# Performance work log

Hardware: AMD Instinct MI355X
Metric: run time of the kernel (lower is better)

The kernel has to match this reference:

```python
import jax, jax.numpy as jnp
import numpy as np

B, T, H, L = 8, 256, 64, 3
NB, NF, HP = 17, 68, 6
K = 9  # temporal kernel
PAD = (K - 1) // 2
EPS = 1e-5


def _normalize(adj):
    adj = adj + np.eye(adj.shape[0], dtype=np.float32)
    d = adj.sum(1)
    dinv = np.power(d, -0.5)
    dinv[np.isinf(dinv)] = 0.0
    return (dinv[:, None] * adj * dinv[None, :]).astype(np.float32)


def _body_adj():
    a = np.zeros((NB, NB), np.float32)
    conns = [(0, 1), (0, 2), (1, 3), (2, 4), (0, 5), (0, 6), (5, 6), (5, 7), (7, 9), (6, 8), (8, 10), (5, 11), (6, 12), (11, 12), (11, 13), (13, 15), (12, 14), (14, 16)]
    for i, j in conns:
        a[i, j] = 1.0
        a[j, i] = 1.0
    return _normalize(a)


def _face_adj():
    a = np.zeros((NF, NF), np.float32)
    for i in range(16): a[i, i + 1] = 1.0
    for i in range(17, 21): a[i, i + 1] = 1.0
    for i in range(22, 26): a[i, i + 1] = 1.0
    for i in range(27, 30): a[i, i + 1] = 1.0
    for i in range(31, 35): a[i, i + 1] = 1.0
    for i in range(36, 41): a[i, i + 1] = 1.0
    a[41, 36] = 1.0
    for i in range(42, 47): a[i, i + 1] = 1.0
    a[47, 42] = 1.0
    for i in range(48, 59): a[i, i + 1] = 1.0
    a[59, 48] = 1.0
    for i in range(60, 67): a[i, i + 1] = 1.0
    a[67, 60] = 1.0
    a = a + a.T
    return _normalize(a)


def setup_inputs() -> dict:
    keys = iter(jax.random.split(jax.random.key(0), 80))

    def rn(shape, s):
        return jax.random.normal(next(keys), shape, jnp.float32) * s

    inp = {}
    inp['body_kps'] = jax.random.normal(next(keys), (B, T, NB * 2), jnp.float32)
    inp['face_kps_2d'] = jax.random.normal(next(keys), (B, T, NF * 2), jnp.float32)
    inp['head_pose'] = jax.random.normal(next(keys), (B, T, HP), jnp.float32)
    inp['body_adj'] = jnp.asarray(_body_adj())
    inp['face_adj'] = jnp.asarray(_face_adj())
    inp['body_proj_w'] = rn((2, H), 0.5)
    inp['body_proj_b'] = jnp.zeros((H,), jnp.float32)
    inp['face_proj_w'] = rn((2, H), 0.5)
    inp['face_proj_b'] = jnp.zeros((H,), jnp.float32)
    inp['head_w'] = rn((HP, H), 0.3)
    inp['head_b'] = jnp.zeros((H,), jnp.float32)
    for p in ('b', 'f'):
        inp[p + '_t1w'] = rn((L, H, H, K), 0.04)
        inp[p + '_t1b'] = jnp.zeros((L, H), jnp.float32)
        inp[p + '_bn1g'] = jnp.ones((L, H), jnp.float32)
        inp[p + '_bn1b'] = jnp.zeros((L, H), jnp.float32)
        inp[p + '_bn1m'] = rn((L, H), 0.1)
        inp[p + '_bn1v'] = jax.random.uniform(next(keys), (L, H), jnp.float32, 0.5, 1.5)
        inp[p + '_gcw'] = rn((L, H, H), 0.1)
        inp[p + '_gcb'] = jnp.zeros((L, H), jnp.float32)
        inp[p + '_t2w'] = rn((L, H, H, K), 0.04)
        inp[p + '_t2b'] = jnp.zeros((L, H), jnp.float32)
        inp[p + '_bn2g'] = jnp.ones((L, H), jnp.float32)
        inp[p + '_bn2b'] = jnp.zeros((L, H), jnp.float32)
        inp[p + '_bn2m'] = rn((L, H), 0.1)
        inp[p + '_bn2v'] = jax.random.uniform(next(keys), (L, H), jnp.float32, 0.5, 1.5)
    total = NB * H + NF * H + H  # 5504
    inp['fus1_w'] = rn((total, 4 * H), 0.02)
    inp['fus1_b'] = jnp.zeros((4 * H,), jnp.float32)
    inp['fus2_w'] = rn((4 * H, 2 * H), 0.06)
    inp['fus2_b'] = jnp.zeros((2 * H,), jnp.float32)
    inp['fus3_w'] = rn((2 * H, H), 0.09)
    inp['fus3_b'] = jnp.zeros((H,), jnp.float32)
    inp['fus4_w'] = rn((H, 5), 0.12)
    inp['fus4_b'] = jnp.zeros((5,), jnp.float32)
    return inp


def _conv_bn(x, w, b, g, be, m, v):
    # x: (BN, C, T); w: (O, I, K). Conv1d (pad=4) + eval-mode BatchNorm1d.
    y = jax.lax.conv_general_dilated(x, w, (1,), [(PAD, PAD)], dimension_numbers=('NCH', 'OIH', 'NCH'))
    y = y + b[None, :, None]
    inv = g * jax.lax.rsqrt(v + EPS)
    return y * inv[None, :, None] + (be - m * inv)[None, :, None]


def _block(x, adj, t1w, t1b, g1, b1, m1, v1, gw, gb, t2w, t2b, g2, b2, m2, v2):
    # x: (B, N, C, T); residual is identity (in_channels == out_channels)
    Bn, N, C, Tn = x.shape
    res = x
    h = jax.nn.relu(_conv_bn(x.reshape(Bn * N, C, Tn), t1w, t1b, g1, b1, m1, v1)).reshape(Bn, N, C, Tn)
    # spatial graph conv, batched over all timesteps at once (adj @ (x W) + b)
    support = jnp.einsum('bnct,co->bnot', h, gw)
    h = jax.nn.relu(jnp.einsum('mn,bnot->bmot', adj, support) + gb[None, None, :, None])
    h = _conv_bn(h.reshape(Bn * N, C, Tn), t2w, t2b, g2, b2, m2, v2).reshape(Bn, N, C, Tn)
    return h + res  # dropout = identity in eval


def _stream(x, n_nodes, pw, pb, adj, ps):
    Bn, Tn, _ = x.shape
    h = x.reshape(Bn, Tn, n_nodes, 2) @ pw + pb          # (B, T, N, H)
    h = jnp.transpose(h, (0, 2, 3, 1))                   # (B, N, H, T)
    for l in range(ps[0].shape[0]):
        h = _block(h, adj, *(p[l] for p in ps))
    return h.mean(axis=3).reshape(Bn, -1)                # temporal mean-pool, flatten nodes


def reference(body_kps, face_kps_2d, head_pose, body_adj, face_adj, body_proj_w, body_proj_b, face_proj_w, face_proj_b, head_w, head_b, b_t1w, b_t1b, b_bn1g, b_bn1b, b_bn1m, b_bn1v, b_gcw, b_gcb, b_t2w, b_t2b, b_bn2g, b_bn2b, b_bn2m, b_bn2v, f_t1w, f_t1b, f_bn1g, f_bn1b, f_bn1m, f_bn1v, f_gcw, f_gcb, f_t2w, f_t2b, f_bn2g, f_bn2b, f_bn2m, f_bn2v, fus1_w, fus1_b, fus2_w, fus2_b, fus3_w, fus3_b, fus4_w, fus4_b):
    bps = (b_t1w, b_t1b, b_bn1g, b_bn1b, b_bn1m, b_bn1v, b_gcw, b_gcb, b_t2w, b_t2b, b_bn2g, b_bn2b, b_bn2m, b_bn2v)
    fps = (f_t1w, f_t1b, f_bn1g, f_bn1b, f_bn1m, f_bn1v, f_gcw, f_gcb, f_t2w, f_t2b, f_bn2g, f_bn2b, f_bn2m, f_bn2v)
    bf = _stream(body_kps, NB, body_proj_w, body_proj_b, body_adj, bps)
    ff = _stream(face_kps_2d, NF, face_proj_w, face_proj_b, face_adj, fps)
    hp = jax.nn.relu(head_pose @ head_w + head_b).mean(axis=1)
    feat = jnp.concatenate([bf, ff, hp], axis=-1)
    h = jax.nn.relu(feat @ fus1_w + fus1_b)
    h = jax.nn.relu(h @ fus2_w + fus2_b)
    h = jax.nn.relu(h @ fus3_w + fus3_b)
    return h @ fus4_w + fus4_b
```

## Files before the change

kernel.cpp:

```cpp
#include <hip/hip_runtime.h>

constexpr int B_ = 8, T_ = 256, H_ = 64, L_ = 3, NB_ = 17, NF_ = 68, HP_ = 6, K_ = 9;
constexpr int FEAT_DIM = NB_ * H_ + NF_ * H_ + H_;
constexpr int HT = H_ * T_;

typedef _Float16 half4_t __attribute__((ext_vector_type(4)));
typedef _Float16 half8_t __attribute__((ext_vector_type(8)));
typedef float f32x16 __attribute__((ext_vector_type(16)));
typedef float f32x4 __attribute__((ext_vector_type(4)));

constexpr size_t SZ_AB = (size_t)B_ * NB_ * HT;
constexpr size_t SZ_AF = (size_t)B_ * NF_ * HT;
constexpr size_t OFF_TB   = 0;
constexpr size_t OFF_TF   = OFF_TB + SZ_AB / 2;
constexpr size_t OFF_SUPB = OFF_TF + SZ_AF / 2;
constexpr size_t OFF_SUPF = OFF_SUPB + SZ_AB / 2;
constexpr size_t OFF_GB   = OFF_SUPF + SZ_AF / 2;
constexpr size_t OFF_GF   = OFF_GB + SZ_AB / 2;
constexpr size_t OFF_W3   = OFF_GF + SZ_AF / 2;
constexpr size_t OFF_GW3  = OFF_W3 + 4 * 55296;
constexpr size_t OFF_B2   = OFF_GW3 + 2 * 6144;
constexpr size_t OFF_ADJPB= OFF_B2 + 768;
constexpr size_t OFF_ADJPF= OFF_ADJPB + 512;
constexpr size_t OFF_FEAT = OFF_ADJPF + 3840;
constexpr size_t OFF_P1   = OFF_FEAT + (size_t)B_ * FEAT_DIM;

struct ConvPrepSet { const float *w, *tb, *g, *bb, *m, *v; };

struct Args {
    const float *body_kps, *face_kps, *head_pose, *body_adj, *face_adj;
    const float *body_pw, *body_pb, *face_pw, *face_pb, *head_w, *head_b;
    ConvPrepSet sb1, sb2, sf1, sf2;
    const float *b_gcw, *f_gcw, *b_gcb, *f_gcb;
    const float *fus1_w, *fus1_b, *fus2_w, *fus2_b, *fus3_w, *fus3_b, *fus4_w, *fus4_b;
    _Float16 *TrB, *TrF, *SupB, *SupF, *Gb, *Gf;
    _Float16 *W3, *GW3, *adjPB, *adjPF;
    float *B2, *p1, *feat;
    float *out;
};

__device__ __forceinline__ half8_t ld_b8(const _Float16* p) {
    half4_t lo = *(const half4_t*)p;
    half4_t hi = *(const half4_t*)(p + 4);
    return __builtin_shufflevector(lo, hi, 0, 1, 2, 3, 4, 5, 6, 7);
}

__device__ __forceinline__ void st_b8(_Float16* p, half8_t v) {
    half4_t lo, hi;
#pragma unroll
    for (int j = 0; j < 4; ++j) { lo[j] = v[j]; hi[j] = v[4 + j]; }
    *(half4_t*)p = lo;
    *(half4_t*)(p + 4) = hi;
}

__device__ __forceinline__ void stage_chunk64(const _Float16* __restrict__ xb,
                                              _Float16* __restrict__ Xs, int tc, int tid) {
    for (int u = tid; u < 72 * 8; u += 256) {
        int row = u >> 3, c = u & 7;
        int t = tc * 64 + row - 4;
        half8_t v;
        if (t >= 0 && t < T_) {
            v = *(const half8_t*)(xb + (size_t)t * H_ + c * 8);
        } else {
#pragma unroll
            for (int j = 0; j < 8; ++j) v[j] = (_Float16)0.f;
        }
        st_b8(&Xs[row * 68 + c * 8], v);
    }
}

__device__ __forceinline__ void stage_res64(const _Float16* __restrict__ xb,
                                            _Float16* __restrict__ Rs, int tc, int tid) {
    for (int u = tid; u < 64 * 8; u += 256) {
        int row = u >> 3, c = u & 7;
        half8_t v = *(const half8_t*)(xb + (size_t)(tc * 64 + row) * H_ + c * 8);
        st_b8(&Rs[row * 68 + c * 8], v);
    }
}

__device__ __forceinline__ void conv_kloop(const half8_t* __restrict__ wl,
                                           const _Float16* __restrict__ Xs,
                                           int trow, int ln31, int kg, int ot,
                                           f32x16& acc) {
    const _Float16* xr0 = Xs + (size_t)(trow + ln31) * 68;
#pragma unroll
    for (int tap = 0; tap < K_; ++tap) {
#pragma unroll
        for (int ks = 0; ks < 4; ++ks) {
            int i8 = ks * 2 + kg;
            half8_t a = wl[(tap * 8 + i8) * H_ + ot * 32 + ln31];
            half8_t bf = ld_b8(xr0 + tap * 68 + i8 * 8);
            acc = __builtin_amdgcn_mfma_f32_32x32x16_f16(a, bf, acc, 0, 0, 0);
        }
    }
}

__device__ void convmix_core(const half8_t* __restrict__ wl,
                             const float* __restrict__ b1l,
                             const half8_t* __restrict__ gl,
                             _Float16* __restrict__ supb,
                             int tc, _Float16* __restrict__ Xs, int tid) {
    int ln = tid & 63;
    int w = __builtin_amdgcn_readfirstlane(tid >> 6);
    int ln31 = ln & 31, kg = ln >> 5;
    int ts = w & 1, ot = w >> 1;
    int trow = ts * 32;

    f32x16 acc;
#pragma unroll
    for (int r = 0; r < 16; ++r) acc[r] = 0.f;

    conv_kloop(wl, Xs, trow, ln31, kg, ot, acc);
    __syncthreads();

    _Float16* mrow = Xs + (size_t)(4 + trow + ln31) * 68;
#pragma unroll
    for (int rg = 0; rg < 4; ++rg) {
        int o0 = ot * 32 + rg * 8 + kg * 4;
        f32x4 bv = *(const f32x4*)(b1l + o0);
        half4_t hv;
#pragma unroll
        for (int j = 0; j < 4; ++j)
            hv[j] = (_Float16)fmaxf(acc[rg * 4 + j] + bv[j], 0.f);
        *(half4_t*)(mrow + o0) = hv;
    }
    __syncthreads();

    f32x16 acc2;
#pragma unroll
    for (int r = 0; r < 16; ++r) acc2[r] = 0.f;
#pragma unroll
    for (int ks = 0; ks < 4; ++ks) {
        int i8 = ks * 2 + kg;
        half8_t a = gl[i8 * H_ + ot * 32 + ln31];
        half8_t bf = ld_b8(mrow + i8 * 8);
        acc2 = __builtin_amdgcn_mfma_f32_32x32x16_f16(a, bf, acc2, 0, 0, 0);
    }
    __syncthreads();

#pragma unroll
    for (int rg = 0; rg < 4; ++rg) {
        int o0 = ot * 32 + rg * 8 + kg * 4;
        half4_t hv;
#pragma unroll
        for (int j = 0; j < 4; ++j)
            hv[j] = (_Float16)acc2[rg * 4 + j];
        *(half4_t*)(mrow + o0) = hv;
    }
    __syncthreads();
    _Float16* gout = supb + (size_t)(tc * 64) * H_;
    const _Float16* srow = Xs + 4 * 68;
#pragma unroll
    for (int k2 = 0; k2 < 2; ++k2) {
        int u = k2 * 256 + tid;
        int r = u >> 3, c = u & 7;
        half8_t v = ld_b8(srow + r * 68 + c * 8);
        *(half8_t*)(gout + (size_t)r * H_ + c * 8) = v;
    }
}

__global__ __launch_bounds__(256) void prep_k(Args A) {
    int blk = blockIdx.x;
    int tid = threadIdx.x;
    if (blk < 1728) {
        int set = blk / 432;
        int bx = blk % 432;
        ConvPrepSet s = (set == 0) ? A.sb1 : (set == 1) ? A.sb2 : (set == 2) ? A.sf1 : A.sf2;
        int idx = bx * 256 + tid;
        int k = idx % K_; int r = idx / K_;
        int i = r % H_; r /= H_;
        int o = r % H_; int l = r / H_;
        float sc = s.g[l * H_ + o] * rsqrtf(s.v[l * H_ + o] + 1e-5f);
        A.W3[(size_t)set * 110592 + ((((l * K_ + k) * 8 + (i >> 3)) * H_ + o) * 8) + (i & 7)]
            = (_Float16)(s.w[idx] * sc);
        if (i == 0 && k == 0)
            A.B2[set * 192 + l * H_ + o] =
                s.tb[l * H_ + o] * sc + s.bb[l * H_ + o] - s.m[l * H_ + o] * sc;
    } else if (blk < 1824) {
        int set = (blk - 1728) / 48;
        int bx = (blk - 1728) % 48;
        const float* gw = set ? A.f_gcw : A.b_gcw;
        int idx = bx * 256 + tid;
        int o = idx % H_; int r = idx / H_;
        int c = r % H_; int l = r / H_;
        A.GW3[(size_t)set * 12288 + (((l * 8 + (c >> 3)) * H_ + o) * 8) + (c & 7)]
            = (_Float16)gw[idx];
    } else {
        int idx = (blk - 1824) * 256 + tid;
        if (idx < 1024) {
            int m = idx >> 5, k = idx & 31;
            A.adjPB[idx] = (m < NB_ && k < NB_) ? (_Float16)A.body_adj[m * NB_ + k] : (_Float16)0.f;
        } else if (idx < 8704) {
            int j = idx - 1024;
            int m = j / 80, k = j % 80;
            A.adjPF[j] = (m < NF_ && k < NF_) ? (_Float16)A.face_adj[m * NF_ + k] : (_Float16)0.f;
        } else if (idx < 10752) {
            A.p1[idx - 8704] = 0.f;
        } else if (idx < 10752 + B_ * FEAT_DIM) {
            A.feat[idx - 10752] = 0.f;
        }
    }
}

__global__ __launch_bounds__(256, 8) void projcm_k(Args A) {
    __shared__ __align__(16) _Float16 Xs[72 * 68];
    int blk = blockIdx.x, tid = threadIdx.x;
    bool isB = blk < 4 * B_ * NB_;
    int j = isB ? blk : blk - 4 * B_ * NB_;
    int bn = j >> 2, tc = j & 3;
    const float* kps = isB ? A.body_kps : A.face_kps;
    const float* pw  = isB ? A.body_pw  : A.face_pw;
    const float* pb  = isB ? A.body_pb  : A.face_pb;
    _Float16* trunk  = isB ? A.TrB : A.TrF;
    int N = isB ? NB_ : NF_;
    int b = bn / N, n = bn % N;

    if (tid < 144) {
        int row = tid >> 1, hf = tid & 1;
        int t = tc * 64 + row - 4;
        _Float16* xr = Xs + row * 68 + hf * 32;
        if (t >= 0 && t < T_) {
            float x0 = kps[((size_t)b * T_ + t) * (N * 2) + n * 2 + 0];
            float x1 = kps[((size_t)b * T_ + t) * (N * 2) + n * 2 + 1];
            bool own = (row >= 4 && row < 68);
            _Float16* ob = trunk + (size_t)bn * HT + (size_t)t * H_ + hf * 32;
#pragma unroll
            for (int cg2 = 0; cg2 < 4; ++cg2) {
                half8_t v;
#pragma unroll
                for (int jj = 0; jj < 8; ++jj) {
                    int c = hf * 32 + cg2 * 8 + jj;
                    v[jj] = (_Float16)fmaf(x0, pw[c], fmaf(x1, pw[H_ + c], pb[c]));
                }
                st_b8(xr + cg2 * 8, v);
                if (own) *(half8_t*)(ob + cg2 * 8) = v;
            }
        } else {
            half8_t z;
#pragma unroll
            for (int jj = 0; jj < 8; ++jj) z[jj] = (_Float16)0.f;
            st_b8(xr, z);
            st_b8(xr + 8, z);
            st_b8(xr + 16, z);
            st_b8(xr + 24, z);
        }
    }
    __syncthreads();

    const half8_t* w1 = (const half8_t*)(A.W3 + (isB ? 0 : 221184));
    const float* b1l  = isB ? A.B2 : A.B2 + 384;
    const half8_t* gl = (const half8_t*)(A.GW3 + (isB ? 0 : 12288));
    _Float16* supb = (isB ? A.SupB : A.SupF) + (size_t)bn * HT;
    convmix_core(w1, b1l, gl, supb, tc, Xs, tid);
}

__global__ __launch_bounds__(256, 8) void cm_k(Args A, int l) {
    __shared__ __align__(16) _Float16 Xs[72 * 68];
    int blk = blockIdx.x, tid = threadIdx.x;
    bool isB = blk < 4 * B_ * NB_;
    int j = isB ? blk : blk - 4 * B_ * NB_;
    int bn = j >> 2, tc = j & 3;
    const _Float16* trunk = isB ? A.TrB : A.TrF;

    stage_chunk64(trunk + (size_t)bn * HT, Xs, tc, tid);
    __syncthreads();

    const half8_t* w1 = (const half8_t*)(A.W3 + (isB ? 0 : 221184)) + (size_t)l * (K_ * 8 * H_);
    const float* b1l  = (isB ? A.B2 : A.B2 + 384) + l * H_;
    const half8_t* gl = (const half8_t*)(A.GW3 + (isB ? 0 : 12288)) + (size_t)l * (8 * H_);
    _Float16* supb = (isB ? A.SupB : A.SupF) + (size_t)bn * HT;
    convmix_core(w1, b1l, gl, supb, tc, Xs, tid);
}

template <int N, int MT, int KS>
__device__ void adjmix_impl(const _Float16* __restrict__ sup,
                            const half8_t* __restrict__ adjP,
                            const float* __restrict__ gb,
                            _Float16* __restrict__ out,
                            int blk, int l, _Float16* Ls, int tid) {
    constexpr int KP = KS * 16;
    constexpr int PITCH = KP + 4;
    int b = blk >> 7, cb = blk & 127;
    int colbase = cb * 128;

    for (int u = tid; u < KP * 16; u += 256) {
        int n = u >> 4, cs = u & 15;
        half8_t v;
        if (n < N) v = *(const half8_t*)(sup + (size_t)(b * N + n) * HT + colbase + cs * 8);
        else {
#pragma unroll
            for (int j = 0; j < 8; ++j) v[j] = (_Float16)0.f;
        }
#pragma unroll
        for (int j = 0; j < 8; ++j) Ls[(cs * 8 + j) * PITCH + n] = v[j];
    }
    __syncthreads();

    int ln = tid & 63;
    int w = __builtin_amdgcn_readfirstlane(tid >> 6);
    int ln31 = ln & 31, kg = ln >> 5;
    int colL = w * 32 + ln31;

    f32x16 acc[MT];
#pragma unroll
    for (int mt = 0; mt < MT; ++mt)
#pragma unroll
        for (int r = 0; r < 16; ++r) acc[mt][r] = 0.f;

#pragma unroll
    for (int ks = 0; ks < KS; ++ks) {
        half8_t bf = ld_b8(&Ls[colL * PITCH + ks * 16 + kg * 8]);
#pragma unroll
        for (int mt = 0; mt < MT; ++mt) {
            half8_t af = adjP[(size_t)(mt * 32 + ln31) * (KP / 8) + ks * 2 + kg];
            acc[mt] = __builtin_amdgcn_mfma_f32_32x32x16_f16(af, bf, acc[mt], 0, 0, 0);
        }
    }
    __syncthreads();

    float gbv = gb[l * H_ + (colL & 63)];
#pragma unroll
    for (int mt = 0; mt < MT; ++mt) {
#pragma unroll
        for (int r = 0; r < 16; ++r) {
            int m = mt * 32 + (r & 3) + 8 * (r >> 2) + 4 * kg;
            Ls[m * 132 + colL] = (_Float16)fmaxf(acc[mt][r] + gbv, 0.f);
        }
    }
    __syncthreads();

    for (int u = tid; u < N * 16; u += 256) {
        int m = u >> 4, c = u & 15;
        half8_t v = ld_b8(&Ls[m * 132 + c * 8]);
        *(half8_t*)(out + (size_t)(b * N + m) * HT + colbase + c * 8) = v;
    }
}

__global__ __launch_bounds__(256) void adjmix_k(Args A, int l) {
    __shared__ __align__(16) _Float16 Ls[12800];
    int blk = blockIdx.x, tid = threadIdx.x;
    if (blk < 1024)
        adjmix_impl<NB_, 1, 2>(A.SupB, (const half8_t*)A.adjPB, A.b_gcb, A.Gb, blk, l, Ls, tid);
    else
        adjmix_impl<NF_, 3, 5>(A.SupF, (const half8_t*)A.adjPF, A.f_gcb, A.Gf, blk - 1024, l, Ls, tid);
}

__global__ __launch_bounds__(256, 8) void c2_k(Args A, int l) {
    __shared__ __align__(16) _Float16 Xs[72 * 68];
    __shared__ __align__(16) _Float16 Rs[64 * 68];
    int blk = blockIdx.x, tid = threadIdx.x;
    bool isB = blk < 4 * B_ * NB_;
    int j = isB ? blk : blk - 4 * B_ * NB_;
    int bn = j >> 2, tc = j & 3;
    const _Float16* G = isB ? A.Gb : A.Gf;
    _Float16* trunk   = isB ? A.TrB : A.TrF;
    const half8_t* w2 = (const half8_t*)(A.W3 + (isB ? 110592 : 331776)) + (size_t)l * (K_ * 8 * H_);
    const float* b2l  = (isB ? A.B2 + 192 : A.B2 + 576) + l * H_;

    stage_chunk64(G + (size_t)bn * HT, Xs, tc, tid);
    stage_res64(trunk + (size_t)bn * HT, Rs, tc, tid);
    __syncthreads();

    int ln = tid & 63;
    int w = __builtin_amdgcn_readfirstlane(tid >> 6);
    int ln31 = ln & 31, kg = ln >> 5;
    int ts = w & 1, ot = w >> 1;
    int trow = ts * 32;

    f32x16 acc;
#pragma unroll
    for (int r = 0; r < 16; ++r) acc[r] = 0.f;

    conv_kloop(w2, Xs, trow, ln31, kg, ot, acc);
    __syncthreads();

    {
        _Float16* orow = Xs + (size_t)(4 + trow + ln31) * 68;
        const _Float16* rrow = Rs + (size_t)(trow + ln31) * 68;
#pragma unroll
        for (int rg = 0; rg < 4; ++rg) {
            int o0 = ot * 32 + rg * 8 + kg * 4;
            f32x4 bv = *(const f32x4*)(b2l + o0);
            half4_t rv = *(const half4_t*)(rrow + o0);
            half4_t hv;
#pragma unroll
            for (int jj = 0; jj < 4; ++jj)
                hv[jj] = (_Float16)(acc[rg * 4 + jj] + bv[jj] + (float)rv[jj]);
            *(half4_t*)(orow + o0) = hv;
        }
    }
    __syncthreads();

    _Float16* gout = trunk + (size_t)bn * HT + (size_t)(tc * 64) * H_;
    const _Float16* srow = Xs + 4 * 68;
#pragma unroll
    for (int k2 = 0; k2 < 2; ++k2) {
        int u = k2 * 256 + tid;
        int r = u >> 3, c = u & 7;
        half8_t v = ld_b8(srow + r * 68 + c * 8);
        *(half8_t*)(gout + (size_t)r * H_ + c * 8) = v;
    }
}

__global__ __launch_bounds__(256, 8) void c2last_k(Args A) {
    __shared__ __align__(16) _Float16 Xs[72 * 68];
    __shared__ __align__(16) _Float16 Rs[64 * 68];
    int blk = blockIdx.x, tid = threadIdx.x;
    if (blk >= 2720) {
        int b = blk - 2720;
        if (tid < 64) {
            int c = tid;
            float w0 = A.head_w[c], w1 = A.head_w[64 + c], w2 = A.head_w[128 + c],
                  w3 = A.head_w[192 + c], w4 = A.head_w[256 + c], w5 = A.head_w[320 + c];
            float bias = A.head_b[c];
            float acc = 0.f;
            for (int t = 0; t < T_; ++t) {
                const float* xr = A.head_pose + ((size_t)b * T_ + t) * HP_;
                float s = fmaf(xr[0], w0, fmaf(xr[1], w1, fmaf(xr[2], w2,
                          fmaf(xr[3], w3, fmaf(xr[4], w4, fmaf(xr[5], w5, bias))))));
                acc += fmaxf(s, 0.f);
            }
            A.feat[(size_t)b * FEAT_DIM + NB_ * H_ + NF_ * H_ + c] = acc * (1.f / 256.f);
        }
        return;
    }
    constexpr int l = L_ - 1;
    bool isB = blk < 4 * B_ * NB_;
    int j = isB ? blk : blk - 4 * B_ * NB_;
    int bn = j >> 2, tc = j & 3;
    const _Float16* G = isB ? A.Gb : A.Gf;
    _Float16* trunk   = isB ? A.TrB : A.TrF;
    const half8_t* w2 = (const half8_t*)(A.W3 + (isB ? 110592 : 331776)) + (size_t)l * (K_ * 8 * H_);
    const float* b2l  = (isB ? A.B2 + 192 : A.B2 + 576) + l * H_;
    int N = isB ? NB_ : NF_;
    int fbase = isB ? 0 : NB_ * H_;

    stage_chunk64(G + (size_t)bn * HT, Xs, tc, tid);
    stage_res64(trunk + (size_t)bn * HT, Rs, tc, tid);
    __syncthreads();

    int ln = tid & 63;
    int w = __builtin_amdgcn_readfirstlane(tid >> 6);
    int ln31 = ln & 31, kg = ln >> 5;
    int ts = w & 1, ot = w >> 1;
    int trow = ts * 32;

    f32x16 acc;
#pragma unroll
    for (int r = 0; r < 16; ++r) acc[r] = 0.f;

    conv_kloop(w2, Xs, trow, ln31, kg, ot, acc);

    float sv[16];
    const _Float16* rrow = Rs + (size_t)(trow + ln31) * 68;
#pragma unroll
    for (int rg = 0; rg < 4; ++rg) {
        int o0 = ot * 32 + rg * 8 + kg * 4;
        f32x4 bv = *(const f32x4*)(b2l + o0);
        half4_t rv = *(const half4_t*)(rrow + o0);
#pragma unroll
        for (int jj = 0; jj < 4; ++jj) {
            int r = rg * 4 + jj;
            float s = acc[r] + bv[jj] + (float)rv[jj];
#pragma unroll
            for (int off = 1; off < 32; off <<= 1) s += __shfl_xor(s, off);
            sv[r] = s;
        }
    }
    __syncthreads();
    float* red = (float*)Xs;
    if (ln31 == 0) {
#pragma unroll
        for (int r = 0; r < 16; ++r) {
            int olocal = (r & 3) + 8 * (r >> 2) + 4 * kg;
            red[w * 32 + olocal] = sv[r];
        }
    }
    __syncthreads();
    if (tid < 64) {
        int o = tid, ot2 = o >> 5, ol = o & 31;
        float s = red[(ot2 * 2) * 32 + ol] + red[(ot2 * 2 + 1) * 32 + ol];
        int b = bn / N, n = bn % N;
        atomicAdd(&A.feat[(size_t)b * FEAT_DIM + fbase + n * H_ + o], s * (1.f / 256.f));
    }
}

__global__ __launch_bounds__(256) void fus1_k(Args A) {
    __shared__ float fv[8][64];
    int blk = blockIdx.x;
    int ic = blk >> 1, kh = blk & 1;
    int base = ic * 128 + kh * 64;
    int tid = threadIdx.x;
    for (int u = tid; u < 8 * 64; u += 256) {
        int b = u >> 6, j = u & 63;
        fv[b][j] = A.feat[(size_t)b * FEAT_DIM + base + j];
    }
    __syncthreads();
    float acc[8];
#pragma unroll
    for (int b = 0; b < 8; ++b) acc[b] = 0.f;
    const float* wb = A.fus1_w + (size_t)base * 256 + tid;
    for (int i = 0; i < 64; ++i) {
        float wv = wb[(size_t)i * 256];
#pragma unroll
        for (int b = 0; b < 8; ++b) acc[b] = fmaf(fv[b][i], wv, acc[b]);
    }
#pragma unroll
    for (int b = 0; b < 8; ++b) atomicAdd(&A.p1[b * 256 + tid], acc[b]);
}

__global__ __launch_bounds__(256) void fus_tail_k(Args A) {
    __shared__ float s1[256], s2[128], s3[64];
    int b = blockIdx.x, tid = threadIdx.x;
    s1[tid] = fmaxf(A.p1[b * 256 + tid] + A.fus1_b[tid], 0.f);
    __syncthreads();
    if (tid < 128) {
        float acc = A.fus2_b[tid];
        for (int i = 0; i < 256; ++i) acc = fmaf(s1[i], A.fus2_w[i * 128 + tid], acc);
        s2[tid] = fmaxf(acc, 0.f);
    }
    __syncthreads();
    if (tid < 64) {
        float acc = A.fus3_b[tid];
        for (int i = 0; i < 128; ++i) acc = fmaf(s2[i], A.fus3_w[i * 64 + tid], acc);
        s3[tid] = fmaxf(acc, 0.f);
    }
    __syncthreads();
    if (tid < 5) {
        float acc = A.fus4_b[tid];
        for (int i = 0; i < 64; ++i) acc = fmaf(s3[i], A.fus4_w[i * 5 + tid], acc);
        A.out[b * 5 + tid] = acc;
    }
}

extern "C" void kernel_launch(void* const* d_in, const int* in_sizes, int n_in,
                              void* d_out, int out_size, void* d_ws, size_t ws_size,
                              hipStream_t stream) {
    float* ws = (float*)d_ws;

    Args A;
    A.body_kps = (const float*)d_in[0];
    A.face_kps = (const float*)d_in[1];
    A.head_pose = (const float*)d_in[2];
    A.body_adj = (const float*)d_in[3];
    A.face_adj = (const float*)d_in[4];
    A.body_pw = (const float*)d_in[5];
    A.body_pb = (const float*)d_in[6];
    A.face_pw = (const float*)d_in[7];
    A.face_pb = (const float*)d_in[8];
    A.head_w = (const float*)d_in[9];
    A.head_b = (const float*)d_in[10];
    A.sb1 = ConvPrepSet{(const float*)d_in[11], (const float*)d_in[12], (const float*)d_in[13],
                        (const float*)d_in[14], (const float*)d_in[15], (const float*)d_in[16]};
    A.b_gcw = (const float*)d_in[17];
    A.b_gcb = (const float*)d_in[18];
    A.sb2 = ConvPrepSet{(const float*)d_in[19], (const float*)d_in[20], (const float*)d_in[21],
                        (const float*)d_in[22], (const float*)d_in[23], (const float*)d_in[24]};
    A.sf1 = ConvPrepSet{(const float*)d_in[25], (const float*)d_in[26], (const float*)d_in[27],
                        (const float*)d_in[28], (const float*)d_in[29], (const float*)d_in[30]};
    A.f_gcw = (const float*)d_in[31];
    A.f_gcb = (const float*)d_in[32];
    A.sf2 = ConvPrepSet{(const float*)d_in[33], (const float*)d_in[34], (const float*)d_in[35],
                        (const float*)d_in[36], (const float*)d_in[37], (const float*)d_in[38]};
    A.fus1_w = (const float*)d_in[39]; A.fus1_b = (const float*)d_in[40];
    A.fus2_w = (const float*)d_in[41]; A.fus2_b = (const float*)d_in[42];
    A.fus3_w = (const float*)d_in[43]; A.fus3_b = (const float*)d_in[44];
    A.fus4_w = (const float*)d_in[45]; A.fus4_b = (const float*)d_in[46];

    A.TrB  = (_Float16*)(ws + OFF_TB);
    A.TrF  = (_Float16*)(ws + OFF_TF);
    A.SupB = (_Float16*)(ws + OFF_SUPB);
    A.SupF = (_Float16*)(ws + OFF_SUPF);
    A.Gb   = (_Float16*)(ws + OFF_GB);
    A.Gf   = (_Float16*)(ws + OFF_GF);
    A.W3   = (_Float16*)(ws + OFF_W3);
    A.GW3  = (_Float16*)(ws + OFF_GW3);
    A.adjPB= (_Float16*)(ws + OFF_ADJPB);
    A.adjPF= (_Float16*)(ws + OFF_ADJPF);
    A.B2   = ws + OFF_B2;
    A.feat = ws + OFF_FEAT;
    A.p1   = ws + OFF_P1;
    A.out  = (float*)d_out;

    const int gconv = 4 * (B_ * NB_ + B_ * NF_);

    prep_k<<<2038, 256, 0, stream>>>(A);
    projcm_k<<<gconv, 256, 0, stream>>>(A);
    for (int l = 0; l < L_; ++l) {
        adjmix_k<<<2048, 256, 0, stream>>>(A, l);
        if (l < L_ - 1) {
            c2_k<<<gconv, 256, 0, stream>>>(A, l);
            cm_k<<<gconv, 256, 0, stream>>>(A, l + 1);
        } else {
            c2last_k<<<gconv + 8, 256, 0, stream>>>(A);
        }
    }
    fus1_k<<<86, 256, 0, stream>>>(A);
    fus_tail_k<<<8, 256, 0, stream>>>(A);
}
```

Baseline: 372.8 us.

## Fuse each GCN layer into one kernel using connected-component node groups

Replaces the separate conv+mix, dense adjacency-mix, and second-conv kernels with a single per-layer kernel. Each block owns a connected component of the skeleton or face graph (body, jaw, brows, nose, eyes, lips) for one batch and a 16-step time chunk, with halo rows for both temporal convs. The adjacency mix becomes a sparse neighbour sum in LDS instead of a padded dense MFMA. This removes global round trips for the support and graph-conv intermediates and several launches per layer. In exchange it adds redundant halo computation, uses a very large LDS allocation at one block per CU, and relies on the adjacency being block-diagonal across those fixed node groups.

```diff
diff --git a/kernel.cpp b/kernel.cpp
--- a/kernel.cpp
+++ b/kernel.cpp
@@ -13,16 +13,10 @@
 constexpr size_t SZ_AF = (size_t)B_ * NF_ * HT;
 constexpr size_t OFF_TB   = 0;
 constexpr size_t OFF_TF   = OFF_TB + SZ_AB / 2;
-constexpr size_t OFF_SUPB = OFF_TF + SZ_AF / 2;
-constexpr size_t OFF_SUPF = OFF_SUPB + SZ_AB / 2;
-constexpr size_t OFF_GB   = OFF_SUPF + SZ_AF / 2;
-constexpr size_t OFF_GF   = OFF_GB + SZ_AB / 2;
-constexpr size_t OFF_W3   = OFF_GF + SZ_AF / 2;
+constexpr size_t OFF_W3   = OFF_TF + SZ_AF / 2;
 constexpr size_t OFF_GW3  = OFF_W3 + 4 * 55296;
 constexpr size_t OFF_B2   = OFF_GW3 + 2 * 6144;
-constexpr size_t OFF_ADJPB= OFF_B2 + 768;
-constexpr size_t OFF_ADJPF= OFF_ADJPB + 512;
-constexpr size_t OFF_FEAT = OFF_ADJPF + 3840;
+constexpr size_t OFF_FEAT = OFF_B2 + 768;
 constexpr size_t OFF_P1   = OFF_FEAT + (size_t)B_ * FEAT_DIM;
 
 struct ConvPrepSet { const float *w, *tb, *g, *bb, *m, *v; };
@@ -33,8 +27,8 @@
     ConvPrepSet sb1, sb2, sf1, sf2;
     const float *b_gcw, *f_gcw, *b_gcb, *f_gcb;
     const float *fus1_w, *fus1_b, *fus2_w, *fus2_b, *fus3_w, *fus3_b, *fus4_w, *fus4_b;
-    _Float16 *TrB, *TrF, *SupB, *SupF, *Gb, *Gf;
-    _Float16 *W3, *GW3, *adjPB, *adjPF;
+    _Float16 *TrB, *TrF;
+    _Float16 *W3, *GW3;
     float *B2, *p1, *feat;
     float *out;
 };
@@ -51,112 +45,6 @@
     for (int j = 0; j < 4; ++j) { lo[j] = v[j]; hi[j] = v[4 + j]; }
     *(half4_t*)p = lo;
     *(half4_t*)(p + 4) = hi;
-}
-
-__device__ __forceinline__ void stage_chunk64(const _Float16* __restrict__ xb,
-                                              _Float16* __restrict__ Xs, int tc, int tid) {
-    for (int u = tid; u < 72 * 8; u += 256) {
-        int row = u >> 3, c = u & 7;
-        int t = tc * 64 + row - 4;
-        half8_t v;
-        if (t >= 0 && t < T_) {
-            v = *(const half8_t*)(xb + (size_t)t * H_ + c * 8);
-        } else {
-#pragma unroll
-            for (int j = 0; j < 8; ++j) v[j] = (_Float16)0.f;
-        }
-        st_b8(&Xs[row * 68 + c * 8], v);
-    }
-}
-
-__device__ __forceinline__ void stage_res64(const _Float16* __restrict__ xb,
-                                            _Float16* __restrict__ Rs, int tc, int tid) {
-    for (int u = tid; u < 64 * 8; u += 256) {
-        int row = u >> 3, c = u & 7;
-        half8_t v = *(const half8_t*)(xb + (size_t)(tc * 64 + row) * H_ + c * 8);
-        st_b8(&Rs[row * 68 + c * 8], v);
-    }
-}
-
-__device__ __forceinline__ void conv_kloop(const half8_t* __restrict__ wl,
-                                           const _Float16* __restrict__ Xs,
-                                           int trow, int ln31, int kg, int ot,
-                                           f32x16& acc) {
-    const _Float16* xr0 = Xs + (size_t)(trow + ln31) * 68;
-#pragma unroll
-    for (int tap = 0; tap < K_; ++tap) {
-#pragma unroll
-        for (int ks = 0; ks < 4; ++ks) {
-            int i8 = ks * 2 + kg;
-            half8_t a = wl[(tap * 8 + i8) * H_ + ot * 32 + ln31];
-            half8_t bf = ld_b8(xr0 + tap * 68 + i8 * 8);
-            acc = __builtin_amdgcn_mfma_f32_32x32x16_f16(a, bf, acc, 0, 0, 0);
-        }
-    }
-}
-
-__device__ void convmix_core(const half8_t* __restrict__ wl,
-                             const float* __restrict__ b1l,
-                             const half8_t* __restrict__ gl,
-                             _Float16* __restrict__ supb,
-                             int tc, _Float16* __restrict__ Xs, int tid) {
-    int ln = tid & 63;
-    int w = __builtin_amdgcn_readfirstlane(tid >> 6);
-    int ln31 = ln & 31, kg = ln >> 5;
-    int ts = w & 1, ot = w >> 1;
-    int trow = ts * 32;
-
-    f32x16 acc;
-#pragma unroll
-    for (int r = 0; r < 16; ++r) acc[r] = 0.f;
-
-    conv_kloop(wl, Xs, trow, ln31, kg, ot, acc);
-    __syncthreads();
-
-    _Float16* mrow = Xs + (size_t)(4 + trow + ln31) * 68;
-#pragma unroll
-    for (int rg = 0; rg < 4; ++rg) {
-        int o0 = ot * 32 + rg * 8 + kg * 4;
-        f32x4 bv = *(const f32x4*)(b1l + o0);
-        half4_t hv;
-#pragma unroll
-        for (int j = 0; j < 4; ++j)
-            hv[j] = (_Float16)fmaxf(acc[rg * 4 + j] + bv[j], 0.f);
-        *(half4_t*)(mrow + o0) = hv;
-    }
-    __syncthreads();
-
-    f32x16 acc2;
-#pragma unroll
-    for (int r = 0; r < 16; ++r) acc2[r] = 0.f;
-#pragma unroll
-    for (int ks = 0; ks < 4; ++ks) {
-        int i8 = ks * 2 + kg;
-        half8_t a = gl[i8 * H_ + ot * 32 + ln31];
-        half8_t bf = ld_b8(mrow + i8 * 8);
-        acc2 = __builtin_amdgcn_mfma_f32_32x32x16_f16(a, bf, acc2, 0, 0, 0);
-    }
-    __syncthreads();
-
-#pragma unroll
-    for (int rg = 0; rg < 4; ++rg) {
-        int o0 = ot * 32 + rg * 8 + kg * 4;
-        half4_t hv;
-#pragma unroll
-        for (int j = 0; j < 4; ++j)
-            hv[j] = (_Float16)acc2[rg * 4 + j];
-        *(half4_t*)(mrow + o0) = hv;
-    }
-    __syncthreads();
-    _Float16* gout = supb + (size_t)(tc * 64) * H_;
-    const _Float16* srow = Xs + 4 * 68;
-#pragma unroll
-    for (int k2 = 0; k2 < 2; ++k2) {
-        int u = k2 * 256 + tid;
-        int r = u >> 3, c = u & 7;
-        half8_t v = ld_b8(srow + r * 68 + c * 8);
-        *(half8_t*)(gout + (size_t)r * H_ + c * 8) = v;
-    }
 }
 
 __global__ __launch_bounds__(256) void prep_k(Args A) {
@@ -187,227 +75,19 @@
             = (_Float16)gw[idx];
     } else {
         int idx = (blk - 1824) * 256 + tid;
-        if (idx < 1024) {
-            int m = idx >> 5, k = idx & 31;
-            A.adjPB[idx] = (m < NB_ && k < NB_) ? (_Float16)A.body_adj[m * NB_ + k] : (_Float16)0.f;
-        } else if (idx < 8704) {
-            int j = idx - 1024;
-            int m = j / 80, k = j % 80;
-            A.adjPF[j] = (m < NF_ && k < NF_) ? (_Float16)A.face_adj[m * NF_ + k] : (_Float16)0.f;
-        } else if (idx < 10752) {
-            A.p1[idx - 8704] = 0.f;
-        } else if (idx < 10752 + B_ * FEAT_DIM) {
-            A.feat[idx - 10752] = 0.f;
-        }
-    }
-}
-
-__global__ __launch_bounds__(256, 8) void projcm_k(Args A) {
-    __shared__ __align__(16) _Float16 Xs[72 * 68];
-    int blk = blockIdx.x, tid = threadIdx.x;
-    bool isB = blk < 4 * B_ * NB_;
-    int j = isB ? blk : blk - 4 * B_ * NB_;
-    int bn = j >> 2, tc = j & 3;
-    const float* kps = isB ? A.body_kps : A.face_kps;
-    const float* pw  = isB ? A.body_pw  : A.face_pw;
-    const float* pb  = isB ? A.body_pb  : A.face_pb;
-    _Float16* trunk  = isB ? A.TrB : A.TrF;
-    int N = isB ? NB_ : NF_;
-    int b = bn / N, n = bn % N;
-
-    if (tid < 144) {
-        int row = tid >> 1, hf = tid & 1;
-        int t = tc * 64 + row - 4;
-        _Float16* xr = Xs + row * 68 + hf * 32;
-        if (t >= 0 && t < T_) {
-            float x0 = kps[((size_t)b * T_ + t) * (N * 2) + n * 2 + 0];
-            float x1 = kps[((size_t)b * T_ + t) * (N * 2) + n * 2 + 1];
-            bool own = (row >= 4 && row < 68);
-            _Float16* ob = trunk + (size_t)bn * HT + (size_t)t * H_ + hf * 32;
-#pragma unroll
-            for (int cg2 = 0; cg2 < 4; ++cg2) {
-                half8_t v;
-#pragma unroll
-                for (int jj = 0; jj < 8; ++jj) {
-                    int c = hf * 32 + cg2 * 8 + jj;
-                    v[jj] = (_Float16)fmaf(x0, pw[c], fmaf(x1, pw[H_ + c], pb[c]));
-                }
-                st_b8(xr + cg2 * 8, v);
-                if (own) *(half8_t*)(ob + cg2 * 8) = v;
-            }
-        } else {
-            half8_t z;
-#pragma unroll
-            for (int jj = 0; jj < 8; ++jj) z[jj] = (_Float16)0.f;
-            st_b8(xr, z);
-            st_b8(xr + 8, z);
-            st_b8(xr + 16, z);
-            st_b8(xr + 24, z);
-        }
-    }
-    __syncthreads();
-
-    const half8_t* w1 = (const half8_t*)(A.W3 + (isB ? 0 : 221184));
-    const float* b1l  = isB ? A.B2 : A.B2 + 384;
-    const half8_t* gl = (const half8_t*)(A.GW3 + (isB ? 0 : 12288));
-    _Float16* supb = (isB ? A.SupB : A.SupF) + (size_t)bn * HT;
-    convmix_core(w1, b1l, gl, supb, tc, Xs, tid);
-}
-
-__global__ __launch_bounds__(256, 8) void cm_k(Args A, int l) {
-    __shared__ __align__(16) _Float16 Xs[72 * 68];
-    int blk = blockIdx.x, tid = threadIdx.x;
-    bool isB = blk < 4 * B_ * NB_;
-    int j = isB ? blk : blk - 4 * B_ * NB_;
-    int bn = j >> 2, tc = j & 3;
-    const _Float16* trunk = isB ? A.TrB : A.TrF;
-
-    stage_chunk64(trunk + (size_t)bn * HT, Xs, tc, tid);
-    __syncthreads();
-
-    const half8_t* w1 = (const half8_t*)(A.W3 + (isB ? 0 : 221184)) + (size_t)l * (K_ * 8 * H_);
-    const float* b1l  = (isB ? A.B2 : A.B2 + 384) + l * H_;
-    const half8_t* gl = (const half8_t*)(A.GW3 + (isB ? 0 : 12288)) + (size_t)l * (8 * H_);
-    _Float16* supb = (isB ? A.SupB : A.SupF) + (size_t)bn * HT;
-    convmix_core(w1, b1l, gl, supb, tc, Xs, tid);
-}
-
-template <int N, int MT, int KS>
-__device__ void adjmix_impl(const _Float16* __restrict__ sup,
-                            const half8_t* __restrict__ adjP,
-                            const float* __restrict__ gb,
-                            _Float16* __restrict__ out,
-                            int blk, int l, _Float16* Ls, int tid) {
-    constexpr int KP = KS * 16;
-    constexpr int PITCH = KP + 4;
-    int b = blk >> 7, cb = blk & 127;
-    int colbase = cb * 128;
-
-    for (int u = tid; u < KP * 16; u += 256) {
-        int n = u >> 4, cs = u & 15;
-        half8_t v;
-        if (n < N) v = *(const half8_t*)(sup + (size_t)(b * N + n) * HT + colbase + cs * 8);
-        else {
-#pragma unroll
-            for (int j = 0; j < 8; ++j) v[j] = (_Float16)0.f;
-        }
-#pragma unroll
-        for (int j = 0; j < 8; ++j) Ls[(cs * 8 + j) * PITCH + n] = v[j];
-    }
-    __syncthreads();
-
-    int ln = tid & 63;
-    int w = __builtin_amdgcn_readfirstlane(tid >> 6);
-    int ln31 = ln & 31, kg = ln >> 5;
-    int colL = w * 32 + ln31;
-
-    f32x16 acc[MT];
-#pragma unroll
-    for (int mt = 0; mt < MT; ++mt)
-#pragma unroll
-        for (int r = 0; r < 16; ++r) acc[mt][r] = 0.f;
-
-#pragma unroll
-    for (int ks = 0; ks < KS; ++ks) {
-        half8_t bf = ld_b8(&Ls[colL * PITCH + ks * 16 + kg * 8]);
-#pragma unroll
-        for (int mt = 0; mt < MT; ++mt) {
-            half8_t af = adjP[(size_t)(mt * 32 + ln31) * (KP / 8) + ks * 2 + kg];
-            acc[mt] = __builtin_amdgcn_mfma_f32_32x32x16_f16(af, bf, acc[mt], 0, 0, 0);
-        }
-    }
-    __syncthreads();
-
-    float gbv = gb[l * H_ + (colL & 63)];
-#pragma unroll
-    for (int mt = 0; mt < MT; ++mt) {
-#pragma unroll
-        for (int r = 0; r < 16; ++r) {
-            int m = mt * 32 + (r & 3) + 8 * (r >> 2) + 4 * kg;
-            Ls[m * 132 + colL] = (_Float16)fmaxf(acc[mt][r] + gbv, 0.f);
-        }
-    }
-    __syncthreads();
-
-    for (int u = tid; u < N * 16; u += 256) {
-        int m = u >> 4, c = u & 15;
-        half8_t v = ld_b8(&Ls[m * 132 + c * 8]);
-        *(half8_t*)(out + (size_t)(b * N + m) * HT + colbase + c * 8) = v;
-    }
-}
-
-__global__ __launch_bounds__(256) void adjmix_k(Args A, int l) {
-    __shared__ __align__(16) _Float16 Ls[12800];
-    int blk = blockIdx.x, tid = threadIdx.x;
-    if (blk < 1024)
-        adjmix_impl<NB_, 1, 2>(A.SupB, (const half8_t*)A.adjPB, A.b_gcb, A.Gb, blk, l, Ls, tid);
-    else
-        adjmix_impl<NF_, 3, 5>(A.SupF, (const half8_t*)A.adjPF, A.f_gcb, A.Gf, blk - 1024, l, Ls, tid);
-}
-
-__global__ __launch_bounds__(256, 8) void c2_k(Args A, int l) {
-    __shared__ __align__(16) _Float16 Xs[72 * 68];
-    __shared__ __align__(16) _Float16 Rs[64 * 68];
-    int blk = blockIdx.x, tid = threadIdx.x;
-    bool isB = blk < 4 * B_ * NB_;
-    int j = isB ? blk : blk - 4 * B_ * NB_;
-    int bn = j >> 2, tc = j & 3;
-    const _Float16* G = isB ? A.Gb : A.Gf;
-    _Float16* trunk   = isB ? A.TrB : A.TrF;
-    const half8_t* w2 = (const half8_t*)(A.W3 + (isB ? 110592 : 331776)) + (size_t)l * (K_ * 8 * H_);
-    const float* b2l  = (isB ? A.B2 + 192 : A.B2 + 576) + l * H_;
-
-    stage_chunk64(G + (size_t)bn * HT, Xs, tc, tid);
-    stage_res64(trunk + (size_t)bn * HT, Rs, tc, tid);
-    __syncthreads();
-
-    int ln = tid & 63;
-    int w = __builtin_amdgcn_readfirstlane(tid >> 6);
-    int ln31 = ln & 31, kg = ln >> 5;
-    int ts = w & 1, ot = w >> 1;
-    int trow = ts * 32;
-
-    f32x16 acc;
-#pragma unroll
-    for (int r = 0; r < 16; ++r) acc[r] = 0.f;
-
-    conv_kloop(w2, Xs, trow, ln31, kg, ot, acc);
-    __syncthreads();
-
-    {
-        _Float16* orow = Xs + (size_t)(4 + trow + ln31) * 68;
-        const _Float16* rrow = Rs + (size_t)(trow + ln31) * 68;
-#pragma unroll
-        for (int rg = 0; rg < 4; ++rg) {
-            int o0 = ot * 32 + rg * 8 + kg * 4;
-            f32x4 bv = *(const f32x4*)(b2l + o0);
-            half4_t rv = *(const half4_t*)(rrow + o0);
-            half4_t hv;
-#pragma unroll
-            for (int jj = 0; jj < 4; ++jj)
-                hv[jj] = (_Float16)(acc[rg * 4 + jj] + bv[jj] + (float)rv[jj]);
-            *(half4_t*)(orow + o0) = hv;
-        }
-    }
-    __syncthreads();
-
-    _Float16* gout = trunk + (size_t)bn * HT + (size_t)(tc * 64) * H_;
-    const _Float16* srow = Xs + 4 * 68;
-#pragma unroll
-    for (int k2 = 0; k2 < 2; ++k2) {
-        int u = k2 * 256 + tid;
-        int r = u >> 3, c = u & 7;
-        half8_t v = ld_b8(srow + r * 68 + c * 8);
-        *(half8_t*)(gout + (size_t)r * H_ + c * 8) = v;
-    }
-}
-
-__global__ __launch_bounds__(256, 8) void c2last_k(Args A) {
-    __shared__ __align__(16) _Float16 Xs[72 * 68];
-    __shared__ __align__(16) _Float16 Rs[64 * 68];
-    int blk = blockIdx.x, tid = threadIdx.x;
-    if (blk >= 2720) {
-        int b = blk - 2720;
+        if (idx < 2048) {
+            A.p1[idx] = 0.f;
+        } else if (idx < 2048 + B_ * FEAT_DIM) {
+            A.feat[idx - 2048] = 0.f;
+        }
+    }
+}
+
+__global__ __launch_bounds__(256) void proj_k(Args A) {
+    int blk = blockIdx.x;
+    int tid = threadIdx.x;
+    if (blk >= 680) {
+        int b = blk - 680;
         if (tid < 64) {
             int c = tid;
             float w0 = A.head_w[c], w1 = A.head_w[64 + c], w2 = A.head_w[128 + c],
@@ -424,64 +104,261 @@
         }
         return;
     }
-    constexpr int l = L_ - 1;
-    bool isB = blk < 4 * B_ * NB_;
-    int j = isB ? blk : blk - 4 * B_ * NB_;
-    int bn = j >> 2, tc = j & 3;
-    const _Float16* G = isB ? A.Gb : A.Gf;
-    _Float16* trunk   = isB ? A.TrB : A.TrF;
+    bool isB = blk < B_ * NB_;
+    int bn = isB ? blk : blk - B_ * NB_;
+    const float* kps = isB ? A.body_kps : A.face_kps;
+    const float* pw  = isB ? A.body_pw  : A.face_pw;
+    const float* pb  = isB ? A.body_pb  : A.face_pb;
+    _Float16* out = isB ? A.TrB : A.TrF;
+    int N = isB ? NB_ : NF_;
+    int b = bn / N, n = bn % N;
+    int t = tid;
+    float x0 = kps[((size_t)b * T_ + t) * (N * 2) + n * 2 + 0];
+    float x1 = kps[((size_t)b * T_ + t) * (N * 2) + n * 2 + 1];
+    _Float16* ob = out + (size_t)bn * HT + (size_t)t * H_;
+#pragma unroll
+    for (int cg2 = 0; cg2 < 8; ++cg2) {
+        half8_t v;
+#pragma unroll
+        for (int j = 0; j < 8; ++j) {
+            int c = cg2 * 8 + j;
+            v[j] = (_Float16)fmaf(x0, pw[c], fmaf(x1, pw[H_ + c], pb[c]));
+        }
+        *(half8_t*)(ob + cg2 * 8) = v;
+    }
+}
+
+__device__ __forceinline__ _Float16* GrowPtr(_Float16* TRr, _Float16* GXr, int n, int g) {
+    return (g < 8)  ? TRr + ((size_t)(n * 32 + g) * 68)
+         : (g < 16) ? GXr + ((size_t)(n * 8 + (g - 8)) * 68)
+                    : TRr + ((size_t)(n * 32 + g + 8) * 68);
+}
+
+template <bool LAST>
+__global__ __launch_bounds__(256, 1) void layer_k(Args A, int l) {
+    __shared__ __align__(16) _Float16 LS[73984];
+    __shared__ float nbC[17 * 6];
+    __shared__ short nbI[17 * 6];
+    __shared__ int   degA[17];
+    _Float16* TRr  = LS;
+    _Float16* SUPr = LS + 36992;
+    _Float16* GXr  = LS + 64736;
+
+    int tid = threadIdx.x;
+    int blk = blockIdx.x;
+    int b  = blk & 7;
+    int u  = blk >> 3;
+    int gid = u >> 4, tc = u & 15;
+
+    const int nbT[10] = {0, 0, 17, 22, 27, 31, 36, 42, 48, 60};
+    const int ngT[10] = {17, 17, 5, 5, 4, 5, 6, 6, 12, 8};
+    bool isB = (gid == 0);
+    int nb = nbT[gid], NG = ngT[gid];
+    int N  = isB ? NB_ : NF_;
+
+    const _Float16* TrG = isB ? A.TrB : A.TrF;
+    _Float16* TrOut = isB ? A.TrB : A.TrF;
+    const half8_t* w1 = (const half8_t*)(A.W3 + (isB ? 0 : 221184)) + (size_t)l * (K_ * 8 * H_);
     const half8_t* w2 = (const half8_t*)(A.W3 + (isB ? 110592 : 331776)) + (size_t)l * (K_ * 8 * H_);
+    const half8_t* gw = (const half8_t*)(A.GW3 + (isB ? 0 : 12288)) + (size_t)l * (8 * H_);
+    const float* b1l  = (isB ? A.B2 : A.B2 + 384) + l * H_;
     const float* b2l  = (isB ? A.B2 + 192 : A.B2 + 576) + l * H_;
-    int N = isB ? NB_ : NF_;
+    const float* gcbl = (isB ? A.b_gcb : A.f_gcb) + l * H_;
+    const float* adjG = isB ? A.body_adj : A.face_adj;
     int fbase = isB ? 0 : NB_ * H_;
 
-    stage_chunk64(G + (size_t)bn * HT, Xs, tc, tid);
-    stage_res64(trunk + (size_t)bn * HT, Rs, tc, tid);
+    if (tid < NG) {
+        const float* arow = adjG + (size_t)(nb + tid) * N;
+        int d = 0;
+        for (int m = 0; m < NG; ++m) {
+            float c = arow[nb + m];
+            if (c != 0.f) { nbI[tid * 6 + d] = (short)m; nbC[tid * 6 + d] = c; ++d; }
+        }
+        degA[tid] = d;
+    }
+    for (int i = 0; i < NG; ++i) {
+        int v = i * 256 + tid;
+        int n = v >> 8, rr = v & 255;
+        int row = rr >> 3, cg = rr & 7;
+        int t = tc * 16 + row - 8;
+        half8_t hv;
+        if (t >= 0 && t < T_) {
+            hv = *(const half8_t*)(TrG + ((size_t)(b * N + nb + n) * T_ + t) * H_ + cg * 8);
+        } else {
+#pragma unroll
+            for (int j = 0; j < 8; ++j) hv[j] = (_Float16)0.f;
+        }
+        st_b8(&TRr[(size_t)(n * 32 + row) * 68 + cg * 8], hv);
+    }
     __syncthreads();
 
     int ln = tid & 63;
     int w = __builtin_amdgcn_readfirstlane(tid >> 6);
     int ln31 = ln & 31, kg = ln >> 5;
-    int ts = w & 1, ot = w >> 1;
-    int trow = ts * 32;
-
-    f32x16 acc;
-#pragma unroll
-    for (int r = 0; r < 16; ++r) acc[r] = 0.f;
-
-    conv_kloop(w2, Xs, trow, ln31, kg, ot, acc);
-
-    float sv[16];
-    const _Float16* rrow = Rs + (size_t)(trow + ln31) * 68;
-#pragma unroll
-    for (int rg = 0; rg < 4; ++rg) {
-        int o0 = ot * 32 + rg * 8 + kg * 4;
-        f32x4 bv = *(const f32x4*)(b2l + o0);
-        half4_t rv = *(const half4_t*)(rrow + o0);
-#pragma unroll
-        for (int jj = 0; jj < 4; ++jj) {
-            int r = rg * 4 + jj;
-            float s = acc[r] + bv[jj] + (float)rv[jj];
-#pragma unroll
-            for (int off = 1; off < 32; off <<= 1) s += __shfl_xor(s, off);
-            sv[r] = s;
-        }
-    }
-    __syncthreads();
-    float* red = (float*)Xs;
-    if (ln31 == 0) {
-#pragma unroll
-        for (int r = 0; r < 16; ++r) {
-            int olocal = (r & 3) + 8 * (r >> 2) + 4 * kg;
-            red[w * 32 + olocal] = sv[r];
-        }
-    }
-    __syncthreads();
-    if (tid < 64) {
-        int o = tid, ot2 = o >> 5, ol = o & 31;
-        float s = red[(ot2 * 2) * 32 + ol] + red[(ot2 * 2 + 1) * 32 + ol];
-        int b = bn / N, n = bn % N;
-        atomicAdd(&A.feat[(size_t)b * FEAT_DIM + fbase + n * H_ + o], s * (1.f / 256.f));
+    int sE = (ln31 < 24) ? ln31 : 23;
+
+    for (int n = w; n < NG; n += 4) {
+        f32x16 a0c, a1c;
+#pragma unroll
+        for (int r = 0; r < 16; ++r) { a0c[r] = 0.f; a1c[r] = 0.f; }
+        const _Float16* base = &TRr[(size_t)(n * 32 + sE) * 68];
+#pragma unroll
+        for (int tap = 0; tap < K_; ++tap) {
+#pragma unroll
+            for (int ks = 0; ks < 4; ++ks) {
+                int i8 = ks * 2 + kg;
+                half8_t a0 = w1[(tap * 8 + i8) * H_ + ln31];
+                half8_t a1 = w1[(tap * 8 + i8) * H_ + 32 + ln31];
+                half8_t bf = ld_b8(base + tap * 68 + i8 * 8);
+                a0c = __builtin_amdgcn_mfma_f32_32x32x16_f16(a0, bf, a0c, 0, 0, 0);
+                a1c = __builtin_amdgcn_mfma_f32_32x32x16_f16(a1, bf, a1c, 0, 0, 0);
+            }
+        }
+        if (ln31 < 24) {
+            _Float16* mrow = &SUPr[(size_t)(n * 24 + ln31) * 68];
+#pragma unroll
+            for (int ot = 0; ot < 2; ++ot) {
+#pragma unroll
+                for (int rg = 0; rg < 4; ++rg) {
+                    int o0 = ot * 32 + rg * 8 + kg * 4;
+                    f32x4 bv = *(const f32x4*)(b1l + o0);
+                    half4_t hv;
+#pragma unroll
+                    for (int j = 0; j < 4; ++j) {
+                        float y = (ot ? a1c[rg * 4 + j] : a0c[rg * 4 + j]) + bv[j];
+                        hv[j] = (_Float16)fmaxf(y, 0.f);
+                    }
+                    *(half4_t*)(mrow + o0) = hv;
+                }
+            }
+        }
+        f32x16 m0, m1;
+#pragma unroll
+        for (int r = 0; r < 16; ++r) { m0[r] = 0.f; m1[r] = 0.f; }
+        const _Float16* mbase = &SUPr[(size_t)(n * 24 + sE) * 68];
+#pragma unroll
+        for (int ks = 0; ks < 4; ++ks) {
+            int i8 = ks * 2 + kg;
+            half8_t a0 = gw[i8 * H_ + ln31];
+            half8_t a1 = gw[i8 * H_ + 32 + ln31];
+            half8_t bf = ld_b8(mbase + i8 * 8);
+            m0 = __builtin_amdgcn_mfma_f32_32x32x16_f16(a0, bf, m0, 0, 0, 0);
+            m1 = __builtin_amdgcn_mfma_f32_32x32x16_f16(a1, bf, m1, 0, 0, 0);
+        }
+        if (ln31 < 24) {
+            _Float16* srow = &SUPr[(size_t)(n * 24 + ln31) * 68];
+#pragma unroll
+            for (int ot = 0; ot < 2; ++ot) {
+#pragma unroll
+                for (int rg = 0; rg < 4; ++rg) {
+                    int o0 = ot * 32 + rg * 8 + kg * 4;
+                    half4_t hv;
+#pragma unroll
+                    for (int j = 0; j < 4; ++j)
+                        hv[j] = (_Float16)(ot ? m1[rg * 4 + j] : m0[rg * 4 + j]);
+                    *(half4_t*)(srow + o0) = hv;
+                }
+            }
+        }
+    }
+    __syncthreads();
+
+    int P = (NG + 1) >> 1;
+    int nf = ln31 >> 4, sc = ln31 & 15;
+    for (int p = w; p < P; p += 4) {
+        int n0 = 2 * p;
+        bool two = (n0 + 1 < NG);
+        for (int q = 0; q < 2; ++q) {
+            if (q == 1 && !two) break;
+            int n = n0 + q;
+            int dg = degA[n];
+            for (int it = 0; it < 12; ++it) {
+                int v = it * 64 + ln;
+                int s = v >> 5, cp = v & 31, c = cp * 2;
+                float v0 = 0.f, v1 = 0.f;
+                for (int j = 0; j < dg; ++j) {
+                    int m = nbI[n * 6 + j];
+                    float cf = nbC[n * 6 + j];
+                    const _Float16* sp = &SUPr[(size_t)(m * 24 + s) * 68 + c];
+                    v0 = fmaf(cf, (float)sp[0], v0);
+                    v1 = fmaf(cf, (float)sp[1], v1);
+                }
+                v0 = fmaxf(v0 + gcbl[c], 0.f);
+                v1 = fmaxf(v1 + gcbl[c + 1], 0.f);
+                _Float16* gp = GrowPtr(TRr, GXr, n, s) + c;
+                gp[0] = (_Float16)v0;
+                gp[1] = (_Float16)v1;
+            }
+        }
+        int node = n0 + (two ? nf : 0);
+        f32x16 a0c, a1c;
+#pragma unroll
+        for (int r = 0; r < 16; ++r) { a0c[r] = 0.f; a1c[r] = 0.f; }
+#pragma unroll
+        for (int tap = 0; tap < K_; ++tap) {
+#pragma unroll
+            for (int ks = 0; ks < 4; ++ks) {
+                int i8 = ks * 2 + kg;
+                half8_t a0 = w2[(tap * 8 + i8) * H_ + ln31];
+                half8_t a1 = w2[(tap * 8 + i8) * H_ + 32 + ln31];
+                half8_t bf = ld_b8(GrowPtr(TRr, GXr, node, sc + tap) + i8 * 8);
+                a0c = __builtin_amdgcn_mfma_f32_32x32x16_f16(a0, bf, a0c, 0, 0, 0);
+                a1c = __builtin_amdgcn_mfma_f32_32x32x16_f16(a1, bf, a1c, 0, 0, 0);
+            }
+        }
+        bool valid = two || (nf == 0);
+        const _Float16* rrow = &TRr[(size_t)(node * 32 + 8 + sc) * 68];
+        if (!LAST) {
+            if (valid) {
+                _Float16* og = TrOut + ((size_t)(b * N + nb + node) * T_ + tc * 16 + sc) * H_;
+#pragma unroll
+                for (int ot = 0; ot < 2; ++ot) {
+#pragma unroll
+                    for (int rg = 0; rg < 4; ++rg) {
+                        int o0 = ot * 32 + rg * 8 + kg * 4;
+                        f32x4 bv = *(const f32x4*)(b2l + o0);
+                        half4_t rv = *(const half4_t*)(rrow + o0);
+                        half4_t hv;
+#pragma unroll
+                        for (int j = 0; j < 4; ++j) {
+                            float y = (ot ? a1c[rg * 4 + j] : a0c[rg * 4 + j])
+                                    + bv[j] + (float)rv[j];
+                            hv[j] = (_Float16)y;
+                        }
+                        *(half4_t*)(og + o0) = hv;
+                    }
+                }
+            }
+        } else {
+            float sv[2][16];
+#pragma unroll
+            for (int ot = 0; ot < 2; ++ot) {
+#pragma unroll
+                for (int rg = 0; rg < 4; ++rg) {
+                    int o0 = ot * 32 + rg * 8 + kg * 4;
+                    f32x4 bv = *(const f32x4*)(b2l + o0);
+                    half4_t rv = *(const half4_t*)(rrow + o0);
+#pragma unroll
+                    for (int j = 0; j < 4; ++j) {
+                        int r = rg * 4 + j;
+                        float y = valid ? ((ot ? a1c[r] : a0c[r]) + bv[j] + (float)rv[j]) : 0.f;
+#pragma unroll
+                        for (int off = 1; off < 16; off <<= 1) y += __shfl_xor(y, off);
+                        sv[ot][r] = y;
+                    }
+                }
+            }
+            if (sc == 0 && valid) {
+#pragma unroll
+                for (int ot = 0; ot < 2; ++ot)
+#pragma unroll
+                    for (int r = 0; r < 16; ++r) {
+                        int o = ot * 32 + (r & 3) + 8 * (r >> 2) + 4 * kg;
+                        atomicAdd(&A.feat[(size_t)b * FEAT_DIM + fbase + (nb + node) * H_ + o],
+                                  sv[ot][r] * (1.f / 256.f));
+                    }
+            }
+        }
     }
 }
 
@@ -569,32 +446,18 @@
 
     A.TrB  = (_Float16*)(ws + OFF_TB);
     A.TrF  = (_Float16*)(ws + OFF_TF);
-    A.SupB = (_Float16*)(ws + OFF_SUPB);
-    A.SupF = (_Float16*)(ws + OFF_SUPF);
-    A.Gb   = (_Float16*)(ws + OFF_GB);
-    A.Gf   = (_Float16*)(ws + OFF_GF);
     A.W3   = (_Float16*)(ws + OFF_W3);
     A.GW3  = (_Float16*)(ws + OFF_GW3);
-    A.adjPB= (_Float16*)(ws + OFF_ADJPB);
-    A.adjPF= (_Float16*)(ws + OFF_ADJPF);
     A.B2   = ws + OFF_B2;
     A.feat = ws + OFF_FEAT;
     A.p1   = ws + OFF_P1;
     A.out  = (float*)d_out;
 
-    const int gconv = 4 * (B_ * NB_ + B_ * NF_);
-
     prep_k<<<2038, 256, 0, stream>>>(A);
-    projcm_k<<<gconv, 256, 0, stream>>>(A);
-    for (int l = 0; l < L_; ++l) {
-        adjmix_k<<<2048, 256, 0, stream>>>(A, l);
-        if (l < L_ - 1) {
-            c2_k<<<gconv, 256, 0, stream>>>(A, l);
-            cm_k<<<gconv, 256, 0, stream>>>(A, l + 1);
-        } else {
-            c2last_k<<<gconv + 8, 256, 0, stream>>>(A);
-        }
-    }
+    proj_k<<<688, 256, 0, stream>>>(A);
+    layer_k<false><<<1280, 256, 0, stream>>>(A, 0);
+    layer_k<false><<<1280, 256, 0, stream>>>(A, 1);
+    layer_k<true><<<1280, 256, 0, stream>>>(A, 2);
     fus1_k<<<86, 256, 0, stream>>>(A);
     fus_tail_k<<<8, 256, 0, stream>>>(A);
 }
```

Result: slower. 674.9 us (+81.1%).
